# Kernel tuning notes

Hardware: AMD Instinct MI355X
Metric: run time of the kernel (lower is better)

Reference implementation:

```python
import jax, jax.numpy as jnp
import numpy as np

NUM_EMBEDDING = 8192
EMBEDDING_DIM = 512
BS = 16384
NEG_SLOPE = 0.01  # torch LeakyReLU default


def setup_inputs() -> dict:
    key = jax.random.key(0)
    k1, k2, k3, k4, k5, k6, k7 = jax.random.split(key, 7)
    d, K = EMBEDDING_DIM, NUM_EMBEDDING
    s1 = 1.0 / np.sqrt(d)
    return {
        "encoded_eeg": jax.random.normal(k1, (BS, d), dtype=jnp.float32),
        "encoded_mel": jax.random.normal(k2, (BS, d), dtype=jnp.float32),
        "embeddings": jax.random.normal(k3, (K, d), dtype=jnp.float32),
        "W1": jax.random.uniform(k4, (d, d), jnp.float32, -s1, s1),
        "b1": jax.random.uniform(k5, (d,), jnp.float32, -s1, s1),
        "W2": jax.random.uniform(k6, (K, d), jnp.float32, -s1, s1),
        "b2": jax.random.uniform(k7, (K,), jnp.float32, -s1, s1),
    }


def reference(encoded_eeg, encoded_mel, embeddings, W1, b1, W2, b2):
    # --- nearest-codebook indices for mel (detached in original) ---
    flat_mel = encoded_mel.reshape(-1, EMBEDDING_DIM)
    dists = (jnp.sum(embeddings ** 2, axis=1)[None, :]
             + jnp.sum(flat_mel ** 2, axis=1, keepdims=True)
             - 2.0 * flat_mel @ embeddings.T)  # [BS, K]
    mel_indices = jnp.argmin(dists, axis=-1)  # [BS]

    # --- small MLP logits over eeg ---
    flat_eeg = encoded_eeg.reshape(-1, EMBEDDING_DIM)
    h = flat_eeg @ W1.T + b1
    h = jnp.where(h >= 0, h, NEG_SLOPE * h)  # LeakyReLU
    logits = h @ W2.T + b2  # [BS, K]

    eeg_indices = jnp.argmax(logits, axis=-1)
    acc_rate = jnp.mean((eeg_indices == mel_indices).astype(jnp.float32))

    # cross entropy (mean over batch)
    logp = jax.nn.log_softmax(logits, axis=-1)
    loss = -jnp.mean(jnp.take_along_axis(logp, mel_indices[:, None], axis=1))
    return (loss, acc_rate)
```

## Files before the change

kernel.cpp:

```cpp
#include <hip/hip_runtime.h>
#include <hip/hip_bf16.h>
#include <hip/hip_fp8.h>

#define BSZ 16384
#define DIM 512
#define NEMB 8192
#define NEG 0.01f
#define NSPLIT 8

typedef __attribute__((ext_vector_type(8))) short short8;
typedef __attribute__((ext_vector_type(4))) float f32x4;
typedef __attribute__((ext_vector_type(4))) int i32x4;
typedef __attribute__((ext_vector_type(8))) int i32x8;

typedef const __attribute__((address_space(1))) void GVT;
typedef __attribute__((address_space(3))) void LVT;

__device__ __forceinline__ void gl_lds16(const void* g, void* l) {
    __builtin_amdgcn_global_load_lds((GVT*)g, (LVT*)l, 16, 0, 0);
}

__device__ __forceinline__ float bf2f(unsigned short u) {
    union { unsigned int i; float f; } c; c.i = ((unsigned int)u) << 16; return c.f;
}
__device__ __forceinline__ unsigned short f2bf(float f) {
    union { __hip_bfloat16 h; unsigned short u; } c; c.h = __float2bfloat16(f); return c.u;
}
__device__ __forceinline__ unsigned char f2fp8(float f) {
    __hip_fp8_e4m3 t(f); return (unsigned char)t.__x;
}
__device__ __forceinline__ unsigned int fkey(float f) {
    unsigned int u = __float_as_uint(f);
    return u ^ ((unsigned int)((int)u >> 31) | 0x80000000u);
}

__device__ __forceinline__ size_t pack_addr(int r, int k) {
    int kg = k >> 6, ko = k & 63;
    int half = ko >> 5, lq = (ko & 31) >> 3, sub = ko & 7;
    int L = lq * 16 + (r & 15);
    return ((size_t)((r >> 4) * 8 + kg) << 10) + (size_t)(L << 4) + (half << 3) + sub;
}

#define EPILOGUE(NT) do { \
    int c0off = (NT) << 6; \
    if (is_logits) { \
        _Pragma("unroll") for (int ni = 0; ni < 4; ni++) { \
            int j = c0off + ni * 16 + l15; \
            float bb = sAux[j]; \
            unsigned int ic = (unsigned int)(NEMB - 1 - (nbase + j)); \
            _Pragma("unroll") for (int mi = 0; mi < 2; mi++) \
                _Pragma("unroll") for (int rg = 0; rg < 4; rg++) { \
                    float logit = acc[mi][ni][rg] + bb; \
                    int r = mi * 4 + rg; \
                    s[r] += __expf(logit); \
                    unsigned int pk = (fkey(logit) & 0xFFFFE000u) | ic; \
                    pbest[r] = pbest[r] > pk ? pbest[r] : pk; \
                    acc[mi][ni][rg] = 0.f; \
                } \
        } \
    } else { \
        _Pragma("unroll") for (int ni = 0; ni < 4; ni++) { \
            int j = c0off + ni * 16 + l15; \
            float en = sAux[j]; \
            unsigned int cl = (unsigned int)(nbase + j); \
            _Pragma("unroll") for (int mi = 0; mi < 2; mi++) \
                _Pragma("unroll") for (int rg = 0; rg < 4; rg++) { \
                    float d = fmaf(-2.f, acc[mi][ni][rg], en); \
                    unsigned int pk = (fkey(d) & 0xFFFFE000u) | cl; \
                    int r = mi * 4 + rg; \
                    pbest[r] = pbest[r] < pk ? pbest[r] : pk; \
                    acc[mi][ni][rg] = 0.f; \
                } \
        } \
    } \
} while (0)

__global__ void k_prep(const float* __restrict__ eeg, const float* __restrict__ mel,
                       const float* __restrict__ emb, const float* __restrict__ W2,
                       const float* __restrict__ W1,
                       unsigned short* __restrict__ o_eeg, unsigned short* __restrict__ o_w1,
                       unsigned char* __restrict__ o_mel8, unsigned char* __restrict__ o_emb8,
                       unsigned char* __restrict__ o_w28,
                       float* __restrict__ enorm,
                       float* __restrict__ acc2, int* __restrict__ cnt) {
    int bid = blockIdx.x, tid = threadIdx.x;
    if (bid == 0 && tid == 0) { acc2[0] = 0.f; acc2[1] = 0.f; *cnt = 0; }
    if (bid < 1024) {
        const int n_big = BSZ * DIM / 4;
        const int n_mid = NEMB * DIM / 4;
        const int n_w1  = DIM * DIM / 4;
        const int total = n_big * 2 + n_mid * 2 + n_w1;
        for (int i = bid * 256 + tid; i < total; i += 1024 * 256) {
            int j = i;
            if (j < n_big) {
                float4 v = ((const float4*)eeg)[j];
                ushort4 o; o.x = f2bf(v.x); o.y = f2bf(v.y); o.z = f2bf(v.z); o.w = f2bf(v.w);
                ((ushort4*)o_eeg)[j] = o;
            } else if ((j -= n_big) < n_w1) {
                float4 v = ((const float4*)W1)[j];
                ushort4 o; o.x = f2bf(v.x); o.y = f2bf(v.y); o.z = f2bf(v.z); o.w = f2bf(v.w);
                ((ushort4*)o_w1)[j] = o;
            } else if ((j -= n_w1) < n_big) {
                float4 v = ((const float4*)mel)[j];
                uchar4 o; o.x = f2fp8(v.x); o.y = f2fp8(v.y); o.z = f2fp8(v.z); o.w = f2fp8(v.w);
                *(uchar4*)(o_mel8 + pack_addr(j >> 7, (j & 127) * 4)) = o;
            } else if ((j -= n_big) < n_mid) {
                float4 v = ((const float4*)emb)[j];
                uchar4 o; o.x = f2fp8(v.x); o.y = f2fp8(v.y); o.z = f2fp8(v.z); o.w = f2fp8(v.w);
                *(uchar4*)(o_emb8 + pack_addr(j >> 7, (j & 127) * 4)) = o;
            } else {
                j -= n_mid;
                float4 v = ((const float4*)W2)[j];
                uchar4 o; o.x = f2fp8(v.x); o.y = f2fp8(v.y); o.z = f2fp8(v.z); o.w = f2fp8(v.w);
                *(uchar4*)(o_w28 + pack_addr(j >> 7, (j & 127) * 4)) = o;
            }
        }
    } else {
        int w = tid >> 6, lane = tid & 63;
        int row0 = (bid - 1024) * 8 + w * 2;
        #pragma unroll
        for (int t = 0; t < 2; t++) {
            int row = row0 + t;
            const float4* p = (const float4*)(emb + (size_t)row * DIM) + lane * 2;
            float4 a = p[0], b = p[1];
            float s = a.x*a.x + a.y*a.y + a.z*a.z + a.w*a.w
                    + b.x*b.x + b.y*b.y + b.z*b.z + b.w*b.w;
            #pragma unroll
            for (int d = 1; d < 64; d <<= 1) s += __shfl_xor(s, d);
            if (lane == 0) enorm[row] = s;
        }
    }
}

__launch_bounds__(256, 2)
__global__ void k_hgemm(const unsigned short* __restrict__ A,
                        const unsigned short* __restrict__ B,
                        const float* __restrict__ b1,
                        unsigned short* __restrict__ H,
                        unsigned char* __restrict__ H8) {
    __shared__ __align__(16) unsigned short sA[4096], sB[4096];
    int tid = threadIdx.x;
    int w = tid >> 6, lane = tid & 63;
    int wr = w >> 1, wc = w & 1;
    int lquad = lane >> 4, l15 = lane & 15;
    int mt = blockIdx.x >> 2, nt = blockIdx.x & 3;
    int m0 = mt * 128, n0 = nt * 128;

    int e0 = w * 512 + lane * 8;
    int r0 = e0 >> 5, ce = e0 & 31;
    const unsigned short* gA0 = A + (m0 + r0) * DIM + ce;
    const unsigned short* gA1 = gA0 + 64 * DIM;
    const unsigned short* gB0 = B + (n0 + r0) * DIM + ce;
    const unsigned short* gB1 = gB0 + 64 * DIM;
    unsigned short* lA0 = sA + w * 512;  unsigned short* lA1 = sA + (w + 4) * 512;
    unsigned short* lB0 = sB + w * 512;  unsigned short* lB1 = sB + (w + 4) * 512;

    int offA[4], offB[4];
    #pragma unroll
    for (int i = 0; i < 4; i++) {
        offA[i] = (wr * 64 + i * 16 + l15) * 32 + lquad * 8;
        offB[i] = (wc * 64 + i * 16 + l15) * 32 + lquad * 8;
    }

    f32x4 acc[4][4];
    #pragma unroll
    for (int mi = 0; mi < 4; mi++)
        #pragma unroll
        for (int ni = 0; ni < 4; ni++) acc[mi][ni] = 0;

    for (int kk = 0; kk < 16; kk++) {
        gl_lds16(gA0, lA0); gl_lds16(gA1, lA1);
        gl_lds16(gB0, lB0); gl_lds16(gB1, lB1);
        gA0 += 32; gA1 += 32; gB0 += 32; gB1 += 32;
        __syncthreads();
        short8 af[4], bf_[4];
        #pragma unroll
        for (int i = 0; i < 4; i++) {
            af[i]  = *(const short8*)&sA[offA[i]];
            bf_[i] = *(const short8*)&sB[offB[i]];
        }
        #pragma unroll
        for (int mi = 0; mi < 4; mi++)
            #pragma unroll
            for (int ni = 0; ni < 4; ni++)
                acc[mi][ni] = __builtin_amdgcn_mfma_f32_16x16x32_bf16(af[mi], bf_[ni], acc[mi][ni], 0, 0, 0);
        __syncthreads();
    }

    #pragma unroll
    for (int ni = 0; ni < 4; ni++) {
        int col = n0 + wc * 64 + ni * 16 + l15;
        float bv = b1[col];
        #pragma unroll
        for (int mi = 0; mi < 4; mi++) {
            int rowb = m0 + wr * 64 + mi * 16 + lquad * 4;
            #pragma unroll
            for (int rg = 0; rg < 4; rg++) {
                float v = acc[mi][ni][rg] + bv;
                v = v >= 0.f ? v : NEG * v;
                H[(rowb + rg) * DIM + col] = f2bf(v);
                H8[pack_addr(rowb + rg, col)] = f2fp8(v);
            }
        }
    }
}

__launch_bounds__(256, 3)
__global__ void k_big(const unsigned char* __restrict__ Mel8,
                      const unsigned char* __restrict__ Emb8,
                      const unsigned char* __restrict__ H8,
                      const unsigned char* __restrict__ W28,
                      const float* __restrict__ enorm,
                      const float* __restrict__ b2,
                      float* __restrict__ p_s,
                      unsigned int* __restrict__ p_pmax,
                      unsigned int* __restrict__ p_pmin) {
    __shared__ float sAux[1024];
    int tid = threadIdx.x;
    int w = tid >> 6, lane = tid & 63;
    int lquad = lane >> 4, l15 = lane & 15;
    int bid = blockIdx.x;
    int split = bid & 7;
    int is_logits = (bid >> 3) & 1;
    int mt = bid >> 4;
    int m0 = mt * 128, nbase = split * (NEMB / NSPLIT);

    const unsigned char* gAb = (is_logits ? H8 : Mel8);
    const unsigned char* gBb = (is_logits ? W28 : Emb8);

    #pragma unroll
    for (int j = 0; j < 4; j++) {
        int c = tid + j * 256;
        sAux[c] = is_logits ? b2[nbase + c] : (enorm[nbase + c] - 512.0f);
    }

    i32x8 fa8[2][4];
    #pragma unroll
    for (int mi = 0; mi < 2; mi++)
        #pragma unroll
        for (int kp = 0; kp < 4; kp++) {
            const unsigned char* p = gAb
                + ((size_t)(((m0 >> 4) + 2 * w + mi) * 8 + 2 * kp) << 10) + lane * 16;
            i32x4 lo = *(const i32x4*)p;
            i32x4 hi = *(const i32x4*)(p + 1024);
            fa8[mi][kp] = __builtin_shufflevector(lo, hi, 0, 1, 2, 3, 4, 5, 6, 7);
        }
    __syncthreads();

    const unsigned char* gB0 = gBb + (((size_t)(nbase >> 4) * 8) << 10) + lane * 16;

    f32x4 acc[2][4];
    #pragma unroll
    for (int mi = 0; mi < 2; mi++)
        #pragma unroll
        for (int ni = 0; ni < 4; ni++) acc[mi][ni] = 0;

    float s[8];
    unsigned int pbest[8];
    unsigned int pinit = is_logits ? 0u : 0xFFFFFFFFu;
    #pragma unroll
    for (int r = 0; r < 8; r++) { s[r] = 0.f; pbest[r] = pinit; }

    for (int nt = 0; nt < 16; nt++) {
        const unsigned char* pB = gB0 + (size_t)nt * 32768;
        #pragma unroll
        for (int kp = 0; kp < 4; kp++) {
            i32x8 fb[4];
            #pragma unroll
            for (int ni = 0; ni < 4; ni++) {
                const unsigned char* q = pB + ni * 8192 + kp * 2048;
                i32x4 lo = *(const i32x4*)q;
                i32x4 hi = *(const i32x4*)(q + 1024);
                fb[ni] = __builtin_shufflevector(lo, hi, 0, 1, 2, 3, 4, 5, 6, 7);
            }
            __builtin_amdgcn_s_setprio(1);
            #pragma unroll
            for (int mi = 0; mi < 2; mi++)
                #pragma unroll
                for (int ni = 0; ni < 4; ni++)
                    acc[mi][ni] = __builtin_amdgcn_mfma_scale_f32_16x16x128_f8f6f4(
                        fa8[mi][kp], fb[ni], acc[mi][ni], 0, 0, 0, 0x7F7F7F7Fu, 0, 0x7F7F7F7Fu);
            __builtin_amdgcn_s_setprio(0);
        }
        EPILOGUE(nt);
    }

    if (is_logits) {
        #pragma unroll
        for (int r = 0; r < 8; r++)
            #pragma unroll
            for (int d = 1; d < 16; d <<= 1) {
                s[r] += __shfl_xor(s[r], d);
                unsigned int o = (unsigned int)__shfl_xor((int)pbest[r], d);
                pbest[r] = pbest[r] > o ? pbest[r] : o;
            }
        if (l15 == 0) {
            #pragma unroll
            for (int mi = 0; mi < 2; mi++)
                #pragma unroll
                for (int rg = 0; rg < 4; rg++) {
                    int row = w * 32 + mi * 16 + lquad * 4 + rg;
                    int pidx = split * BSZ + m0 + row;
                    p_s[pidx] = s[mi * 4 + rg];
                    p_pmax[pidx] = pbest[mi * 4 + rg];
                }
        }
    } else {
        #pragma unroll
        for (int r = 0; r < 8; r++)
            #pragma unroll
            for (int d = 1; d < 16; d <<= 1) {
                unsigned int o = (unsigned int)__shfl_xor((int)pbest[r], d);
                pbest[r] = pbest[r] < o ? pbest[r] : o;
            }
        if (l15 == 0) {
            #pragma unroll
            for (int mi = 0; mi < 2; mi++)
                #pragma unroll
                for (int rg = 0; rg < 4; rg++) {
                    int row = w * 32 + mi * 16 + lquad * 4 + rg;
                    p_pmin[split * BSZ + m0 + row] = pbest[mi * 4 + rg];
                }
        }
    }
}

__global__ void k_tail(const float* __restrict__ p_s, const unsigned int* __restrict__ p_pmax,
                       const unsigned int* __restrict__ p_pmin,
                       const unsigned short* __restrict__ H,
                       const float* __restrict__ W2,
                       const float* __restrict__ b2,
                       float* __restrict__ acc2, int* __restrict__ cnt,
                       float* __restrict__ out) {
    __shared__ int s_idx[256];
    __shared__ float s_l1[256], s_match[256];
    __shared__ float s_d[4];
    int bid = blockIdx.x, tid = threadIdx.x;
    int w = tid >> 6, lane = tid & 63;
    int r = bid * 256 + tid;

    float S = 0.f; unsigned int PM = 0u, PN = 0xFFFFFFFFu;
    #pragma unroll
    for (int sp = 0; sp < NSPLIT; sp++) {
        S += p_s[sp * BSZ + r];
        unsigned int a = p_pmax[sp * BSZ + r];
        PM = PM > a ? PM : a;
        unsigned int b = p_pmin[sp * BSZ + r];
        PN = PN < b ? PN : b;
    }
    int eidx = (NEMB - 1) - (int)(PM & 0x1FFFu);
    int midx = (int)(PN & 0x1FFFu);
    s_idx[tid] = midx;
    s_l1[tid] = __logf(S) - b2[midx];
    s_match[tid] = (eidx == midx) ? 1.f : 0.f;
    __syncthreads();

    float d0 = 0.f, d1 = 0.f;
    for (int j = 0; j < 64; j++) {
        int rr = w * 64 + j;
        int ridx = s_idx[rr];
        uint4 hv = *(const uint4*)(H + (size_t)(bid * 256 + rr) * DIM + lane * 8);
        const float4* wp = (const float4*)(W2 + (size_t)ridx * DIM + lane * 8);
        float4 w0 = wp[0], w1 = wp[1];
        float p = bf2f((unsigned short)(hv.x & 0xffff)) * w0.x + bf2f((unsigned short)(hv.x >> 16)) * w0.y
                + bf2f((unsigned short)(hv.y & 0xffff)) * w0.z + bf2f((unsigned short)(hv.y >> 16)) * w0.w
                + bf2f((unsigned short)(hv.z & 0xffff)) * w1.x + bf2f((unsigned short)(hv.z >> 16)) * w1.y
                + bf2f((unsigned short)(hv.w & 0xffff)) * w1.z + bf2f((unsigned short)(hv.w >> 16)) * w1.w;
        if (j & 1) d1 += p; else d0 += p;
    }
    float ds = d0 + d1;
    #pragma unroll
    for (int d = 1; d < 64; d <<= 1) ds += __shfl_xor(ds, d);
    if (lane == 0) s_d[w] = ds;

    __syncthreads();
    for (int st = 128; st > 0; st >>= 1) {
        if (tid < st) { s_l1[tid] += s_l1[tid + st]; s_match[tid] += s_match[tid + st]; }
        __syncthreads();
    }
    if (tid == 0) {
        float loss_blk = s_l1[0] - (s_d[0] + s_d[1] + s_d[2] + s_d[3]);
        atomicAdd(&acc2[0], loss_blk * (1.0f / BSZ));
        atomicAdd(&acc2[1], s_match[0] * (1.0f / BSZ));
        __threadfence();
        if (atomicAdd(cnt, 1) == 63) {
            float L = atomicAdd(&acc2[0], 0.f);
            float M = atomicAdd(&acc2[1], 0.f);
            out[0] = L; out[1] = M;
        }
    }
}

extern "C" void kernel_launch(void* const* d_in, const int* in_sizes, int n_in,
                              void* d_out, int out_size, void* d_ws, size_t ws_size,
                              hipStream_t stream) {
    const float* eeg = (const float*)d_in[0];
    const float* mel = (const float*)d_in[1];
    const float* emb = (const float*)d_in[2];
    const float* W1  = (const float*)d_in[3];
    const float* b1  = (const float*)d_in[4];
    const float* W2  = (const float*)d_in[5];
    const float* b2  = (const float*)d_in[6];
    float* out = (float*)d_out;

    unsigned short* ws_eeg = (unsigned short*)d_ws;
    unsigned short* ws_w1  = ws_eeg + (size_t)BSZ * DIM;
    unsigned short* ws_h   = ws_w1  + (size_t)DIM * DIM;
    unsigned char*  ws_h8  = (unsigned char*)(ws_h + (size_t)BSZ * DIM);
    unsigned char*  ws_mel8 = ws_h8  + (size_t)BSZ * DIM;
    unsigned char*  ws_emb8 = ws_mel8 + (size_t)BSZ * DIM;
    unsigned char*  ws_w28  = ws_emb8 + (size_t)NEMB * DIM;
    float* ws_en  = (float*)(ws_w28 + (size_t)NEMB * DIM);
    float* p_s    = ws_en + NEMB;
    unsigned int* p_pmax = (unsigned int*)(p_s + (size_t)NSPLIT * BSZ);
    unsigned int* p_pmin = p_pmax + (size_t)NSPLIT * BSZ;
    float* acc2   = (float*)(p_pmin + (size_t)NSPLIT * BSZ);
    int*   cnt    = (int*)(acc2 + 2);

    k_prep<<<2048, 256, 0, stream>>>(eeg, mel, emb, W2, W1,
                                     ws_eeg, ws_w1, ws_mel8, ws_emb8, ws_w28,
                                     ws_en, acc2, cnt);
    k_hgemm<<<(BSZ / 128) * (DIM / 128), 256, 0, stream>>>(ws_eeg, ws_w1, b1, ws_h, ws_h8);
    k_big<<<(BSZ / 128) * NSPLIT * 2, 256, 0, stream>>>(ws_mel8, ws_emb8, ws_h8, ws_w28,
                                                        ws_en, b2, p_s, p_pmax, p_pmin);
    k_tail<<<BSZ / 256, 256, 0, stream>>>(p_s, p_pmax, p_pmin, ws_h, W2, b2, acc2, cnt, out);
}
```

Before: 360.4 us.

## Software-pipeline B fragment loads with double buffers and pairwise argmax epilogue

The inner GEMM loop now double-buffers B fragments in registers, issuing the global loads for the next half-tile before the MFMAs on the current one, and prefetching across n-tiles. Accumulators are initialized to zero through the first MFMA's C operand instead of being explicitly reset. The epilogue reduces the four column candidates per row pairwise before packing into the key, which cuts the number of key/compare operations. This aims to hide global load latency behind matrix ops, at the cost of more live registers and a redundant prefetch on the last iteration.

```diff
diff --git a/kernel.cpp b/kernel.cpp
--- a/kernel.cpp
+++ b/kernel.cpp
@@ -41,37 +41,64 @@
     return ((size_t)((r >> 4) * 8 + kg) << 10) + (size_t)(L << 4) + (half << 3) + sub;
 }
 
+#define LOADG(BUF, BASE, KP, P) do { \
+    const unsigned char* q0_ = (BASE) + (2 * (P)) * 8192 + (KP) * 2048; \
+    ((i32x4*)&BUF[0])[0] = *(const i32x4*)q0_; \
+    ((i32x4*)&BUF[0])[1] = *(const i32x4*)(q0_ + 1024); \
+    ((i32x4*)&BUF[1])[0] = *(const i32x4*)(q0_ + 8192); \
+    ((i32x4*)&BUF[1])[1] = *(const i32x4*)(q0_ + 8192 + 1024); \
+} while (0)
+
+#define MFMAG(BUF, KP, P, FIRST) do { \
+    __builtin_amdgcn_s_setprio(1); \
+    _Pragma("unroll") for (int mi = 0; mi < 2; mi++) { \
+        f32x4 c0_ = (FIRST) ? Z4 : acc[mi][2 * (P)]; \
+        f32x4 c1_ = (FIRST) ? Z4 : acc[mi][2 * (P) + 1]; \
+        acc[mi][2 * (P)]     = __builtin_amdgcn_mfma_scale_f32_16x16x128_f8f6f4( \
+            fa8[mi][KP], BUF[0], c0_, 0, 0, 0, 0x7F7F7F7Fu, 0, 0x7F7F7F7Fu); \
+        acc[mi][2 * (P) + 1] = __builtin_amdgcn_mfma_scale_f32_16x16x128_f8f6f4( \
+            fa8[mi][KP], BUF[1], c1_, 0, 0, 0, 0x7F7F7F7Fu, 0, 0x7F7F7F7Fu); \
+    } \
+    __builtin_amdgcn_s_setprio(0); \
+} while (0)
+
 #define EPILOGUE(NT) do { \
-    int c0off = (NT) << 6; \
+    int j0 = ((NT) << 6) + l15; \
     if (is_logits) { \
-        _Pragma("unroll") for (int ni = 0; ni < 4; ni++) { \
-            int j = c0off + ni * 16 + l15; \
-            float bb = sAux[j]; \
-            unsigned int ic = (unsigned int)(NEMB - 1 - (nbase + j)); \
-            _Pragma("unroll") for (int mi = 0; mi < 2; mi++) \
-                _Pragma("unroll") for (int rg = 0; rg < 4; rg++) { \
-                    float logit = acc[mi][ni][rg] + bb; \
-                    int r = mi * 4 + rg; \
-                    s[r] += __expf(logit); \
-                    unsigned int pk = (fkey(logit) & 0xFFFFE000u) | ic; \
-                    pbest[r] = pbest[r] > pk ? pbest[r] : pk; \
-                    acc[mi][ni][rg] = 0.f; \
-                } \
-        } \
+        float bb0 = sAux[j0], bb1 = sAux[j0 + 16], bb2 = sAux[j0 + 32], bb3 = sAux[j0 + 48]; \
+        unsigned int ic0 = (unsigned int)(NEMB - 1 - (nbase + j0)); \
+        _Pragma("unroll") for (int mi = 0; mi < 2; mi++) \
+            _Pragma("unroll") for (int rg = 0; rg < 4; rg++) { \
+                float v0 = acc[mi][0][rg] + bb0; \
+                float v1 = acc[mi][1][rg] + bb1; \
+                float v2 = acc[mi][2][rg] + bb2; \
+                float v3 = acc[mi][3][rg] + bb3; \
+                int r = mi * 4 + rg; \
+                s[r] += (__expf(v0) + __expf(v1)) + (__expf(v2) + __expf(v3)); \
+                float m01 = fmaxf(v0, v1); unsigned int i01 = v1 > v0 ? ic0 - 16 : ic0; \
+                float m23 = fmaxf(v2, v3); unsigned int i23 = v3 > v2 ? ic0 - 48 : ic0 - 32; \
+                unsigned int ii = m23 > m01 ? i23 : i01; \
+                float m = fmaxf(m01, m23); \
+                unsigned int pk = (fkey(m) & 0xFFFFE000u) | ii; \
+                pbest[r] = pbest[r] > pk ? pbest[r] : pk; \
+            } \
     } else { \
-        _Pragma("unroll") for (int ni = 0; ni < 4; ni++) { \
-            int j = c0off + ni * 16 + l15; \
-            float en = sAux[j]; \
-            unsigned int cl = (unsigned int)(nbase + j); \
-            _Pragma("unroll") for (int mi = 0; mi < 2; mi++) \
-                _Pragma("unroll") for (int rg = 0; rg < 4; rg++) { \
-                    float d = fmaf(-2.f, acc[mi][ni][rg], en); \
-                    unsigned int pk = (fkey(d) & 0xFFFFE000u) | cl; \
-                    int r = mi * 4 + rg; \
-                    pbest[r] = pbest[r] < pk ? pbest[r] : pk; \
-                    acc[mi][ni][rg] = 0.f; \
-                } \
-        } \
+        float en0 = sAux[j0], en1 = sAux[j0 + 16], en2 = sAux[j0 + 32], en3 = sAux[j0 + 48]; \
+        unsigned int cl0 = (unsigned int)(nbase + j0); \
+        _Pragma("unroll") for (int mi = 0; mi < 2; mi++) \
+            _Pragma("unroll") for (int rg = 0; rg < 4; rg++) { \
+                float v0 = fmaf(-2.f, acc[mi][0][rg], en0); \
+                float v1 = fmaf(-2.f, acc[mi][1][rg], en1); \
+                float v2 = fmaf(-2.f, acc[mi][2][rg], en2); \
+                float v3 = fmaf(-2.f, acc[mi][3][rg], en3); \
+                float m01 = fminf(v0, v1); unsigned int i01 = v1 < v0 ? cl0 + 16 : cl0; \
+                float m23 = fminf(v2, v3); unsigned int i23 = v3 < v2 ? cl0 + 48 : cl0 + 32; \
+                unsigned int ii = m23 < m01 ? i23 : i01; \
+                float m = fminf(m01, m23); \
+                unsigned int pk = (fkey(m) & 0xFFFFE000u) | ii; \
+                int r = mi * 4 + rg; \
+                pbest[r] = pbest[r] < pk ? pbest[r] : pk; \
+            } \
     } \
 } while (0)
 
@@ -241,19 +268,16 @@
         for (int kp = 0; kp < 4; kp++) {
             const unsigned char* p = gAb
                 + ((size_t)(((m0 >> 4) + 2 * w + mi) * 8 + 2 * kp) << 10) + lane * 16;
-            i32x4 lo = *(const i32x4*)p;
-            i32x4 hi = *(const i32x4*)(p + 1024);
-            fa8[mi][kp] = __builtin_shufflevector(lo, hi, 0, 1, 2, 3, 4, 5, 6, 7);
+            ((i32x4*)&fa8[mi][kp])[0] = *(const i32x4*)p;
+            ((i32x4*)&fa8[mi][kp])[1] = *(const i32x4*)(p + 1024);
         }
     __syncthreads();
 
     const unsigned char* gB0 = gBb + (((size_t)(nbase >> 4) * 8) << 10) + lane * 16;
 
+    const f32x4 Z4 = {0.f, 0.f, 0.f, 0.f};
     f32x4 acc[2][4];
-    #pragma unroll
-    for (int mi = 0; mi < 2; mi++)
-        #pragma unroll
-        for (int ni = 0; ni < 4; ni++) acc[mi][ni] = 0;
+    i32x8 fbA[2], fbB[2];
 
     float s[8];
     unsigned int pbest[8];
@@ -261,27 +285,19 @@
     #pragma unroll
     for (int r = 0; r < 8; r++) { s[r] = 0.f; pbest[r] = pinit; }
 
+    LOADG(fbA, gB0, 0, 0);
+
     for (int nt = 0; nt < 16; nt++) {
-        const unsigned char* pB = gB0 + (size_t)nt * 32768;
-        #pragma unroll
-        for (int kp = 0; kp < 4; kp++) {
-            i32x8 fb[4];
-            #pragma unroll
-            for (int ni = 0; ni < 4; ni++) {
-                const unsigned char* q = pB + ni * 8192 + kp * 2048;
-                i32x4 lo = *(const i32x4*)q;
-                i32x4 hi = *(const i32x4*)(q + 1024);
-                fb[ni] = __builtin_shufflevector(lo, hi, 0, 1, 2, 3, 4, 5, 6, 7);
-            }
-            __builtin_amdgcn_s_setprio(1);
-            #pragma unroll
-            for (int mi = 0; mi < 2; mi++)
-                #pragma unroll
-                for (int ni = 0; ni < 4; ni++)
-                    acc[mi][ni] = __builtin_amdgcn_mfma_scale_f32_16x16x128_f8f6f4(
-                        fa8[mi][kp], fb[ni], acc[mi][ni], 0, 0, 0, 0x7F7F7F7Fu, 0, 0x7F7F7F7Fu);
-            __builtin_amdgcn_s_setprio(0);
-        }
+        const unsigned char* pB  = gB0 + (size_t)nt * 32768;
+        const unsigned char* pBn = gB0 + (size_t)((nt + 1) & 15) * 32768;
+        LOADG(fbB, pB, 0, 1);  MFMAG(fbA, 0, 0, 1);
+        LOADG(fbA, pB, 1, 0);  MFMAG(fbB, 0, 1, 1);
+        LOADG(fbB, pB, 1, 1);  MFMAG(fbA, 1, 0, 0);
+        LOADG(fbA, pB, 2, 0);  MFMAG(fbB, 1, 1, 0);
+        LOADG(fbB, pB, 2, 1);  MFMAG(fbA, 2, 0, 0);
+        LOADG(fbA, pB, 3, 0);  MFMAG(fbB, 2, 1, 0);
+        LOADG(fbB, pB, 3, 1);  MFMAG(fbA, 3, 0, 0);
+        LOADG(fbA, pBn, 0, 0); MFMAG(fbB, 3, 1, 0);
         EPILOGUE(nt);
     }
 
```

Result: slower. 513.9 us (+42.6%).
